# Kernel optimization log

Measured on AMD Instinct MI355X. Metric: run time of the kernel, lower is better.

## Reference

```python
import jax, jax.numpy as jnp
import numpy as np

# 5x5 Sobel kernels (exact constants from the torch module)
_GX5 = np.array([[2.,1.,1e-6,-1.,-2.],[3.,2.,1e-6,-2.,-3.],[4.,3.,0.,-3.,-4.],[3.,2.,1e-6,-2.,-3.],[2.,1.,1e-6,-1.,-2.]], np.float32)
_GY5 = np.array([[2.,3.,4.,3.,2.],[1.,2.,3.,2.,1.],[1e-6,1e-6,1e-6,1e-6,1e-6],[-1.,-2.,-3.,-2.,-1.],[-2.,-3.,-4.,-3.,-2.]], np.float32)


def _sobel(x):  # x: [B,1,H,W] -> [B,2,H,W] (gx, gy)
    k = jnp.stack([jnp.asarray(_GX5), jnp.asarray(_GY5)])[:, None]  # [2,1,5,5]
    return jax.lax.conv_general_dilated(x, k, (1, 1), 'SAME',
                                        dimension_numbers=('NCHW', 'OIHW', 'NCHW'))


def _quantize(gx, gy):
    # OrientQuantize: magnitude + orientation quantized to 8 bins
    div = 3.1416 / 8.0
    mag = jnp.sqrt(gx * gx + gy * gy + 1e-8)
    o = jnp.arctan2(gy, gx)
    conds = [
        (o >= div) & (o < 3 * div),
        (o >= 3 * div) & (o < 5 * div),
        (o >= 5 * div) & (o < 7 * div),
        ((o >= 7 * div) & (o < 8 * div)) | ((o >= -8 * div) & (o < -7 * div)),
        (o >= -7 * div) & (o < -5 * div),
        (o >= -5 * div) & (o < -3 * div),
        (o >= -3 * div) & (o < -div),
        (o >= -div) & (o < div),
    ]
    q = jnp.select(conds, [jnp.full_like(o, float(i)) for i in range(8)], 3.0)
    return mag, q.astype(jnp.int32)


def setup_inputs() -> dict:
    key = jax.random.key(0)
    k1, k2, k3 = jax.random.split(key, 3)
    return {
        'seg_map': jax.random.normal(k1, (2, 21, 256, 256), jnp.float32),
        'dense_ft': jax.random.normal(k2, (2, 256, 256, 256), jnp.float32),
        'mask': jax.random.normal(k3, (2, 21, 256, 256), jnp.float32),
        'label_with_bg': jnp.ones((2, 21), jnp.float32),
    }


def reference(seg_map, dense_ft, mask, label_with_bg):
    BETA, K, STEP = 1000.0, 100, 5
    n, C, h, w = seg_map.shape
    nfg, ch, hw = C - 1, dense_ft.shape[1], h * w

    # ---- Mix_fg: per-class Sobel orientation edges on sharpened softmax ----
    seg = jax.nn.softmax(seg_map * BETA, axis=1)[:, 1:]            # [n,nfg,h,w]
    edges = _sobel(seg.reshape(n * nfg, 1, h, w)).reshape(n, nfg, 2, h, w)
    label_fg = label_with_bg[:, 1:]                                 # [n,nfg]
    edges = edges * label_fg[:, :, None, None, None]
    mag, q = _quantize(edges[:, :, 0], edges[:, :, 1])              # [n,nfg,h,w]

    # ---- boundary pixels: strongest-K edge magnitudes per (b,c) ----
    _, pos = jax.lax.top_k(mag.reshape(n, nfg, hw), K)              # [n,nfg,K]
    o = jnp.take_along_axis(q.reshape(n, nfg, hw), pos, -1) + 1     # 1..8

    # ---- in_out_div: walk STEP pixels along/against gradient orientation ----
    mod4 = ((o % 4) == 0).astype(jnp.int32)
    horiz = ((o == 2) | (o == 6)).astype(jnp.int32)
    p_out = jnp.where(o < 4, STEP * STEP, -STEP)   # (-STEP)**(1+(o<4))
    p_in = jnp.where(o < 4, -STEP, 1)              # (-STEP)**(o<4)
    s_out = jnp.where(o % 2 == 0, -1, 1)           # (-1)**(1+o)
    s_in = -s_out                                   # (-1)**o
    out_idx = pos + p_out * mod4 * w + s_out * horiz
    in_idx = pos + p_in * mod4 * w + s_in * horiz

    def valid(x):
        return (x % (w - 1) != 0) & (x % (w - 1) != 1) & (x > 0) & (x < hw - 1)

    v_out, v_in = valid(out_idx), valid(in_idx)                     # [n,nfg,K] bool
    oi = jnp.clip(out_idx, 0, hw - 1)
    ii = jnp.clip(in_idx, 0, hw - 1)

    # ---- gather features / mask probs at walked positions ----
    dense = jax.nn.softmax(dense_ft, axis=1).reshape(n, ch, hw)
    msk = jax.nn.softmax(mask, axis=1).reshape(n, C, hw)
    b = jnp.arange(n)[:, None, None]
    outs = dense[b, :, oi]                                          # [n,nfg,K,ch]
    ins = jax.lax.stop_gradient(dense[b, :, ii])                    # detached
    outs_m = jax.lax.stop_gradient(msk[b, :, oi])
    ins_m = jax.lax.stop_gradient(msk[b, :, ii])

    sim = jnp.einsum('bcie,bcje->bcij', outs, ins)                  # [n,nfg,K,K]
    sim_m = jnp.einsum('bcie,bcje->bcij', outs_m, ins_m)

    fvi = v_in.astype(sim.dtype)
    fvo = v_out.astype(sim.dtype)
    ci = jnp.maximum(fvi.sum(-1), 1.0)
    co = jnp.maximum(fvo.sum(-1), 1.0)

    def rowmean(s):  # mean over in-samples -> [n,nfg,K]
        return (s * fvi[:, :, None, :]).sum(-1) / ci[..., None]

    def colmean(s):  # mean over out-samples -> [n,nfg,K]
        return (s * fvo[:, :, :, None]).sum(-2) / co[..., None]

    def gmean(s):    # global masked mean -> [n,nfg]
        num = (s * fvo[:, :, :, None] * fvi[:, :, None, :]).sum((-2, -1))
        return num / jnp.maximum(fvo.sum(-1) * fvi.sum(-1), 1.0)

    def beacon(sgn_mask, sgn_dense, vals, v):
        # loss_constructor: signed masked means over FP/FN/TP/TN categories
        def term(cat, sign):
            m = (cat & v).astype(vals.dtype)
            cnt = m.sum(-1)
            return sign * jnp.where(cnt > 0, (vals * m).sum(-1) / jnp.maximum(cnt, 1.0), 0.0)
        FP = sgn_mask & ~sgn_dense
        FN = ~sgn_mask & sgn_dense
        TP = ~sgn_mask & ~sgn_dense
        TN = sgn_mask & sgn_dense
        return term(FP, -1.0) + term(FN, 1.0) + term(TP, 1.0) + term(TN, -1.0)

    g = gmean(sim)
    gm = gmean(sim_m)
    rm, rmm = rowmean(sim), rowmean(sim_m)
    cm, cmm = colmean(sim), colmean(sim_m)
    sgn_rm = jax.lax.stop_gradient(rm) > g[..., None]
    sgn_rmm = rmm > gm[..., None]
    sgn_cm = jax.lax.stop_gradient(cm) > g[..., None]
    sgn_cmm = cmm > gm[..., None]

    loss_bc = beacon(sgn_rmm, sgn_rm, rm, v_out) + beacon(sgn_cmm, sgn_cm, cm, v_in)
    gate = ((v_in.sum(-1) >= 10) & (v_out.sum(-1) >= 10)).astype(loss_bc.dtype)
    gate = gate * (label_fg > 0).astype(loss_bc.dtype)
    return (loss_bc * gate).sum()
```

## Files before the change

### kernel.cpp

```cpp
#include <hip/hip_runtime.h>
#include <math.h>

#define HW 65536
#define WID 256
#define HEI 256
#define NB 2
#define NFG 20
#define NMAP 40
#define CH 256
#define CSEG 21
#define TK 100
#define PARTS 32
#define PARTN (HW / PARTS)
#define RPP (HEI / PARTS)
#define CAND (PARTS * TK)

__device__ __constant__ float c_GX[25] = {
  2.f,1.f,1e-6f,-1.f,-2.f,
  3.f,2.f,1e-6f,-2.f,-3.f,
  4.f,3.f,0.f,-3.f,-4.f,
  3.f,2.f,1e-6f,-2.f,-3.f,
  2.f,1.f,1e-6f,-1.f,-2.f};
__device__ __constant__ float c_GY[25] = {
  2.f,3.f,4.f,3.f,2.f,
  1.f,2.f,3.f,2.f,1.f,
  1e-6f,1e-6f,1e-6f,1e-6f,1e-6f,
  -1.f,-2.f,-3.f,-2.f,-1.f,
  -2.f,-3.f,-4.f,-3.f,-2.f};

__global__ __launch_bounds__(256) void k_seg(const float* __restrict__ seg_map,
                                             double* __restrict__ seg) {
  int idx = blockIdx.x * blockDim.x + threadIdx.x;
  if (idx >= NB * HW) return;
  int b = idx / HW, p = idx % HW;
  double x[CSEG];
  double m = -INFINITY;
  #pragma unroll
  for (int c = 0; c < CSEG; ++c) {
    double v = (double)seg_map[(size_t)(b * CSEG + c) * HW + p] * 1000.0;
    x[c] = v;
    m = fmax(m, v);
  }
  double s = 0.0;
  #pragma unroll
  for (int c = 0; c < CSEG; ++c) {
    double d = x[c] - m;
    double e = (d < -746.0) ? 0.0 : exp(d);
    x[c] = e; s += e;
  }
  #pragma unroll
  for (int c = 1; c < CSEG; ++c)
    seg[(size_t)(b * NFG + (c - 1)) * HW + p] = x[c] / s;
}

__global__ __launch_bounds__(256) void k_sobel_topk(
    const double* __restrict__ seg, const float* __restrict__ label,
    unsigned char* __restrict__ qb,
    unsigned long long* __restrict__ ckey, int* __restrict__ cidx) {
  int mapi = blockIdx.x / PARTS, part = blockIdx.x % PARTS;
  int tid = threadIdx.x;
  int lane = tid & 63, w = tid >> 6;
  int row0 = part * RPP;
  const double* im = seg + (size_t)mapi * HW;

  __shared__ double tile[RPP + 4][WID];
  __shared__ unsigned int hist4[4][256];
  __shared__ int wtot[4];
  __shared__ int s_r, s_cnt, s_bsel;

  for (int r = 0; r < RPP + 4; ++r) {
    int gr = row0 - 2 + r;
    tile[r][tid] = (gr >= 0 && gr < HEI) ? im[gr * WID + tid] : 0.0;
  }
  hist4[0][tid] = 0; hist4[1][tid] = 0; hist4[2][tid] = 0; hist4[3][tid] = 0;
  if (tid == 0) { s_r = TK; s_cnt = 0; }
  __syncthreads();

  int b = mapi / NFG, c = mapi % NFG;
  double lab = (double)label[b * CSEG + c + 1];
  const double DIVQ = 3.1416 / 8.0;
  const double T1 = DIVQ, T3 = 3.0*DIVQ, T5 = 5.0*DIVQ, T7 = 7.0*DIVQ, T8 = 8.0*DIVQ;

  unsigned long long mykey[RPP];
  #pragma unroll
  for (int k = 0; k < RPP; ++k) {
    double gx = 0.0, gy = 0.0;
    #pragma unroll
    for (int dy = 0; dy < 5; ++dy) {
      #pragma unroll
      for (int dx = 0; dx < 5; ++dx) {
        int xx = tid + dx - 2;
        double v = (xx >= 0 && xx < WID) ? tile[k + dy][xx] : 0.0;
        gx += v * (double)c_GX[dy * 5 + dx];
        gy += v * (double)c_GY[dy * 5 + dx];
      }
    }
    gx *= lab; gy *= lab;
    double mg = sqrt(gx * gx + gy * gy + 1e-8);
    double o = atan2(gy, gx);
    int qv;
    if (o >= T1 && o < T3) qv = 0;
    else if (o >= T3 && o < T5) qv = 1;
    else if (o >= T5 && o < T7) qv = 2;
    else if ((o >= T7 && o < T8) || (o >= -T8 && o < -T7)) qv = 3;
    else if (o >= -T7 && o < -T5) qv = 4;
    else if (o >= -T5 && o < -T3) qv = 5;
    else if (o >= -T3 && o < -T1) qv = 6;
    else if (o >= -T1 && o < T1) qv = 7;
    else qv = 3;
    mykey[k] = (unsigned long long)__double_as_longlong(mg);
    qb[(size_t)mapi * HW + (size_t)(row0 + k) * WID + tid] = (unsigned char)qv;
  }
  __syncthreads();
  unsigned long long* sk = (unsigned long long*)&tile[0][0];
  #pragma unroll
  for (int k = 0; k < RPP; ++k) sk[k * WID + tid] = mykey[k];
  __syncthreads();

  unsigned long long pfx = 0ull, msk = 0ull;
  for (int round = 0; round < 8; ++round) {
    int shift = 56 - 8 * round;
    #pragma unroll
    for (int k = 0; k < RPP; ++k) {
      unsigned long long key = mykey[k];
      if ((key & msk) == pfx)
        atomicAdd(&hist4[w][(unsigned int)(key >> shift) & 0xFFu], 1u);
    }
    __syncthreads();
    int r = s_r;
    int cnt = (int)(hist4[0][tid] + hist4[1][tid] + hist4[2][tid] + hist4[3][tid]);
    hist4[0][tid] = 0; hist4[1][tid] = 0; hist4[2][tid] = 0; hist4[3][tid] = 0;
    int v = cnt;
    #pragma unroll
    for (int off = 1; off < 64; off <<= 1) {
      int u = __shfl_down(v, off, 64);
      if (lane + off < 64) v += u;
    }
    if (lane == 0) wtot[w] = v;
    __syncthreads();
    int add = 0;
    for (int ww = w + 1; ww < 4; ++ww) add += wtot[ww];
    v += add;
    if (v >= r && v - cnt < r) { s_bsel = tid; s_r = r - (v - cnt); }
    __syncthreads();
    pfx |= ((unsigned long long)s_bsel << shift);
    msk |= (0xFFull << shift);
  }
  unsigned long long kv = pfx;
  int need_eq = s_r;

  unsigned long long* outk = ckey + (size_t)mapi * CAND + (size_t)part * TK;
  int* outi = cidx + (size_t)mapi * CAND + (size_t)part * TK;
  int gbase = part * PARTN;
  const int CHN = PARTN / 256;
  int base = tid * CHN;
  int myeq = 0;
  for (int k = 0; k < CHN; ++k) {
    unsigned long long key = sk[base + k];
    if (key > kv) {
      int slot = atomicAdd(&s_cnt, 1);
      outk[slot] = key; outi[slot] = gbase + base + k;
    } else if (key == kv) ++myeq;
  }
  int v2 = myeq;
  #pragma unroll
  for (int off = 1; off < 64; off <<= 1) {
    int u = __shfl_up(v2, off, 64);
    if (lane >= off) v2 += u;
  }
  if (lane == 63) wtot[w] = v2;
  __syncthreads();
  int addl = 0;
  for (int ww = 0; ww < w; ++ww) addl += wtot[ww];
  int incl = v2 + addl;
  int rank = incl - myeq;
  int eqtot = wtot[0] + wtot[1] + wtot[2] + wtot[3];
  int lo = eqtot - need_eq;
  int wb = TK - need_eq;
  for (int k = 0; k < CHN; ++k) {
    unsigned long long key = sk[base + k];
    if (key == kv) {
      if (rank >= lo) { outk[wb + rank - lo] = key; outi[wb + rank - lo] = gbase + base + k; }
      ++rank;
    }
  }
}

__global__ __launch_bounds__(256) void k_topk_merge(
    const unsigned long long* __restrict__ ckey,
    const int* __restrict__ cidx, int* __restrict__ pos) {
  int mapi = blockIdx.x, tid = threadIdx.x;
  int lane = tid & 63, w = tid >> 6;
  __shared__ unsigned long long k_[CAND];
  __shared__ int i_[CAND];
  __shared__ int eqi[CAND];
  __shared__ unsigned int hist4[4][256];
  __shared__ int wtot[4];
  __shared__ int s_r, s_cnt, s_eqn, s_bsel;
  for (int c = tid; c < CAND; c += 256) {
    k_[c] = ckey[(size_t)mapi * CAND + c];
    i_[c] = cidx[(size_t)mapi * CAND + c];
  }
  hist4[0][tid] = 0; hist4[1][tid] = 0; hist4[2][tid] = 0; hist4[3][tid] = 0;
  if (tid == 0) { s_r = TK; s_cnt = 0; s_eqn = 0; }
  __syncthreads();
  unsigned long long pfx = 0ull, msk = 0ull;
  for (int round = 0; round < 8; ++round) {
    int shift = 56 - 8 * round;
    for (int c = tid; c < CAND; c += 256) {
      unsigned long long key = k_[c];
      if ((key & msk) == pfx)
        atomicAdd(&hist4[w][(unsigned int)(key >> shift) & 0xFFu], 1u);
    }
    __syncthreads();
    int r = s_r;
    int cnt = (int)(hist4[0][tid] + hist4[1][tid] + hist4[2][tid] + hist4[3][tid]);
    hist4[0][tid] = 0; hist4[1][tid] = 0; hist4[2][tid] = 0; hist4[3][tid] = 0;
    int v = cnt;
    #pragma unroll
    for (int off = 1; off < 64; off <<= 1) {
      int u = __shfl_down(v, off, 64);
      if (lane + off < 64) v += u;
    }
    if (lane == 0) wtot[w] = v;
    __syncthreads();
    int add = 0;
    for (int ww = w + 1; ww < 4; ++ww) add += wtot[ww];
    v += add;
    if (v >= r && v - cnt < r) { s_bsel = tid; s_r = r - (v - cnt); }
    __syncthreads();
    pfx |= ((unsigned long long)s_bsel << shift);
    msk |= (0xFFull << shift);
  }
  unsigned long long kv = pfx;
  int need_eq = s_r;
  for (int c = tid; c < CAND; c += 256) {
    unsigned long long key = k_[c];
    if (key > kv) {
      int slot = atomicAdd(&s_cnt, 1);
      pos[mapi * TK + slot] = i_[c];
    } else if (key == kv) {
      int e = atomicAdd(&s_eqn, 1);
      eqi[e] = i_[c];
    }
  }
  __syncthreads();
  int eqn = s_eqn;
  int wb = TK - need_eq;
  for (int e = tid; e < eqn; e += 256) {
    int myi = eqi[e];
    int bigger = 0;
    for (int f = 0; f < eqn; ++f) bigger += (eqi[f] > myi) ? 1 : 0;
    if (bigger < need_eq) pos[mapi * TK + wb + bigger] = myi;
  }
}

__global__ __launch_bounds__(256) void k_gather(
    const float* __restrict__ dense_ft, const float* __restrict__ maskp,
    const unsigned char* __restrict__ qb, const int* __restrict__ pos,
    double* __restrict__ outs, double* __restrict__ ins,
    double* __restrict__ outs_m, double* __restrict__ ins_m,
    int* __restrict__ voutArr, int* __restrict__ vinArr) {
  int blk = blockIdx.x;
  int mapi = blk / TK, j = blk % TK;
  int b = mapi / NFG;
  int tid = threadIdx.x;
  int lane = tid & 63, w = tid >> 6;
  int p = pos[mapi * TK + j];
  int o = (int)qb[(size_t)mapi * HW + p] + 1;
  int mod4 = ((o & 3) == 0) ? 1 : 0;
  int horiz = (o == 2 || o == 6) ? 1 : 0;
  int po = (o < 4) ? 25 : -5;
  int pi = (o < 4) ? -5 : 1;
  int so = ((o & 1) == 0) ? -1 : 1;
  int si = -so;
  int out_idx = p + po * mod4 * WID + so * horiz;
  int in_idx  = p + pi * mod4 * WID + si * horiz;
  int ro = out_idx % 255; if (ro < 0) ro += 255;
  int ri = in_idx  % 255; if (ri < 0) ri += 255;
  int vo = (ro != 0 && ro != 1 && out_idx > 0 && out_idx < HW - 1) ? 1 : 0;
  int vi = (ri != 0 && ri != 1 && in_idx  > 0 && in_idx  < HW - 1) ? 1 : 0;
  int oi = out_idx < 0 ? 0 : (out_idx > HW - 1 ? HW - 1 : out_idx);
  int ii = in_idx  < 0 ? 0 : (in_idx  > HW - 1 ? HW - 1 : in_idx);
  if (tid == 0) { voutArr[mapi * TK + j] = vo; vinArr[mapi * TK + j] = vi; }

  if (w < 2) {
    int idx = (w == 0) ? oi : ii;
    double x[4];
    double mx = -INFINITY;
    #pragma unroll
    for (int q = 0; q < 4; ++q) {
      x[q] = (double)dense_ft[(size_t)(b * CH + lane + 64 * q) * HW + idx];
      mx = fmax(mx, x[q]);
    }
    #pragma unroll
    for (int off = 1; off < 64; off <<= 1) mx = fmax(mx, __shfl_xor(mx, off, 64));
    double e[4], s = 0.0;
    #pragma unroll
    for (int q = 0; q < 4; ++q) { e[q] = exp(x[q] - mx); s += e[q]; }
    #pragma unroll
    for (int off = 1; off < 64; off <<= 1) s += __shfl_xor(s, off, 64);
    double* dst = ((w == 0) ? outs : ins) + ((size_t)mapi * TK + j) * CH;
    #pragma unroll
    for (int q = 0; q < 4; ++q) dst[lane + 64 * q] = e[q] / s;
  } else {
    int idx = (w == 2) ? oi : ii;
    double y = (lane < CSEG) ? (double)maskp[(size_t)(b * CSEG + lane) * HW + idx]
                             : -INFINITY;
    double mx = y;
    #pragma unroll
    for (int off = 1; off < 64; off <<= 1) mx = fmax(mx, __shfl_xor(mx, off, 64));
    double e = (lane < CSEG) ? exp(y - mx) : 0.0;
    double s = e;
    #pragma unroll
    for (int off = 1; off < 64; off <<= 1) s += __shfl_xor(s, off, 64);
    if (lane < CSEG)
      (((w == 2) ? outs_m : ins_m) + ((size_t)mapi * TK + j) * CSEG)[lane] = e / s;
  }
}

__global__ __launch_bounds__(256) void k_stats(
    const double* __restrict__ outs, const double* __restrict__ ins,
    const double* __restrict__ outs_m, const double* __restrict__ ins_m,
    const int* __restrict__ voutArr, const int* __restrict__ vinArr,
    const float* __restrict__ label, double* __restrict__ lossmap) {
  int mapi = blockIdx.x, tid = threadIdx.x;
  int b = mapi / NFG, c = mapi % NFG;
  __shared__ double fvo[TK], fvi[TK];
  __shared__ double avi[CH], avo[CH], avim[CSEG], avom[CSEG];
  __shared__ double rm[TK], cm[TK], rmm[TK], cmm[TK];
  __shared__ double s_sfvo, s_sfvi;
  if (tid < TK) {
    fvo[tid] = (double)voutArr[mapi * TK + tid];
    fvi[tid] = (double)vinArr[mapi * TK + tid];
  }
  __syncthreads();
  if (tid == 0) {
    double a = 0.0, d = 0.0;
    for (int j2 = 0; j2 < TK; ++j2) { a += fvo[j2]; d += fvi[j2]; }
    s_sfvo = a; s_sfvi = d;
  }
  const double* OUT  = outs   + (size_t)mapi * TK * CH;
  const double* IN   = ins    + (size_t)mapi * TK * CH;
  const double* OUTm = outs_m + (size_t)mapi * TK * CSEG;
  const double* INm  = ins_m  + (size_t)mapi * TK * CSEG;
  {
    double a = 0.0, d = 0.0;
    for (int j2 = 0; j2 < TK; ++j2) {
      a += IN[j2 * CH + tid] * fvi[j2];
      d += OUT[j2 * CH + tid] * fvo[j2];
    }
    avi[tid] = a; avo[tid] = d;
  }
  if (tid < CSEG) {
    double a = 0.0, d = 0.0;
    for (int j2 = 0; j2 < TK; ++j2) {
      a += INm[j2 * CSEG + tid] * fvi[j2];
      d += OUTm[j2 * CSEG + tid] * fvo[j2];
    }
    avim[tid] = a; avom[tid] = d;
  }
  __syncthreads();
  double ci = fmax(s_sfvi, 1.0), co = fmax(s_sfvo, 1.0);
  if (tid < TK) {
    double d1 = 0.0, d2 = 0.0, d3 = 0.0, d4 = 0.0;
    for (int e = 0; e < CH; ++e) { d1 += OUT[tid * CH + e] * avi[e]; d2 += IN[tid * CH + e] * avo[e]; }
    for (int e = 0; e < CSEG; ++e) { d3 += OUTm[tid * CSEG + e] * avim[e]; d4 += INm[tid * CSEG + e] * avom[e]; }
    rm[tid] = d1 / ci; cm[tid] = d2 / co; rmm[tid] = d3 / ci; cmm[tid] = d4 / co;
  }
  __syncthreads();
  if (tid == 0) {
    double g = 0.0, gm = 0.0;
    for (int e = 0; e < CH; ++e) g += avo[e] * avi[e];
    for (int e = 0; e < CSEG; ++e) gm += avom[e] * avim[e];
    double den = fmax(s_sfvo * s_sfvi, 1.0);
    g /= den; gm /= den;
    double loss = 0.0;
    {
      double s[4] = {0, 0, 0, 0}, cn[4] = {0, 0, 0, 0};
      for (int j2 = 0; j2 < TK; ++j2) {
        int smv = rmm[j2] > gm;
        int dmv = rm[j2] > g;
        int cat = smv ? (dmv ? 3 : 0) : (dmv ? 1 : 2);
        s[cat] += rm[j2] * fvo[j2];
        cn[cat] += fvo[j2];
      }
      const double sg[4] = {-1.0, 1.0, 1.0, -1.0};
      for (int t = 0; t < 4; ++t)
        if (cn[t] > 0.0) loss += sg[t] * (s[t] / fmax(cn[t], 1.0));
    }
    {
      double s[4] = {0, 0, 0, 0}, cn[4] = {0, 0, 0, 0};
      for (int j2 = 0; j2 < TK; ++j2) {
        int smv = cmm[j2] > gm;
        int dmv = cm[j2] > g;
        int cat = smv ? (dmv ? 3 : 0) : (dmv ? 1 : 2);
        s[cat] += cm[j2] * fvi[j2];
        cn[cat] += fvi[j2];
      }
      const double sg[4] = {-1.0, 1.0, 1.0, -1.0};
      for (int t = 0; t < 4; ++t)
        if (cn[t] > 0.0) loss += sg[t] * (s[t] / fmax(cn[t], 1.0));
    }
    float lab = label[b * CSEG + c + 1];
    double gate = (s_sfvi >= 10.0 && s_sfvo >= 10.0 && lab > 0.f) ? 1.0 : 0.0;
    lossmap[mapi] = loss * gate;
  }
}

__global__ __launch_bounds__(64) void k_final(const double* __restrict__ lossmap,
                                              float* __restrict__ out) {
  if (threadIdx.x == 0 && blockIdx.x == 0) {
    double s = 0.0;
    for (int i = 0; i < NMAP; ++i) s += lossmap[i];
    out[0] = (float)s;
  }
}

extern "C" void kernel_launch(void* const* d_in, const int* in_sizes, int n_in,
                              void* d_out, int out_size, void* d_ws, size_t ws_size,
                              hipStream_t stream) {
  const float* seg_map  = (const float*)d_in[0];
  const float* dense_ft = (const float*)d_in[1];
  const float* maskp    = (const float*)d_in[2];
  const float* label    = (const float*)d_in[3];
  float* outp = (float*)d_out;

  char* w = (char*)d_ws;
  double* seg = (double*)w;               w += (size_t)NB * NFG * HW * 8;
  double* outs   = (double*)w;            w += (size_t)NMAP * TK * CH * 8;
  double* ins    = (double*)w;            w += (size_t)NMAP * TK * CH * 8;
  double* outs_m = (double*)w;            w += (size_t)NMAP * TK * CSEG * 8;
  double* ins_m  = (double*)w;            w += (size_t)NMAP * TK * CSEG * 8;
  double* lossmap = (double*)w;           w += (size_t)NMAP * 8;
  unsigned long long* ckey = (unsigned long long*)w; w += (size_t)NMAP * CAND * 8;
  int* cidx = (int*)w;                    w += (size_t)NMAP * CAND * 4;
  int* pos  = (int*)w;                    w += (size_t)NMAP * TK * 4;
  int* vout = (int*)w;                    w += (size_t)NMAP * TK * 4;
  int* vin  = (int*)w;                    w += (size_t)NMAP * TK * 4;
  unsigned char* qb = (unsigned char*)w;  w += (size_t)NMAP * HW;

  k_seg<<<(NB * HW + 255) / 256, 256, 0, stream>>>(seg_map, seg);
  k_sobel_topk<<<NMAP * PARTS, 256, 0, stream>>>(seg, label, qb, ckey, cidx);
  k_topk_merge<<<NMAP, 256, 0, stream>>>(ckey, cidx, pos);
  k_gather<<<NMAP * TK, 256, 0, stream>>>(dense_ft, maskp, qb, pos, outs, ins,
                                          outs_m, ins_m, vout, vin);
  k_stats<<<NMAP, 256, 0, stream>>>(outs, ins, outs_m, ins_m, vout, vin, label, lossmap);
  k_final<<<1, 64, 0, stream>>>(lossmap, outp);
}
```

Measured before the change: 199.5 us.

## Speed up radix-select top-k with run-length histogram atomics and early exit

In both the per-part Sobel top-k and the merge kernel, histogram updates now combine consecutive keys that fall in the same bin into one atomic add. Each thread also scans a contiguous chunk of candidates in the merge, so neighbouring keys are more likely to share a bin. The radix rounds stop early once the selected bucket holds a single key. The O(n^2) tie-breaking among equal keys in the merge is replaced by a fast path when all ties are needed, or a two-round radix select on indices. The goal is to cut shared-memory atomic contention and redundant rounds, at the cost of extra branches and a nondeterministic output order for tied entries.

```diff
diff --git a/kernel.cpp b/kernel.cpp
--- a/kernel.cpp
+++ b/kernel.cpp
@@ -14,6 +14,7 @@
 #define PARTN (HW / PARTS)
 #define RPP (HEI / PARTS)
 #define CAND (PARTS * TK)
+#define MCH 13
 
 __device__ __constant__ float c_GX[25] = {
   2.f,1.f,1e-6f,-1.f,-2.f,
@@ -66,7 +67,8 @@
   __shared__ double tile[RPP + 4][WID];
   __shared__ unsigned int hist4[4][256];
   __shared__ int wtot[4];
-  __shared__ int s_r, s_cnt, s_bsel;
+  __shared__ int s_r, s_cnt, s_bsel, s_selcnt;
+  __shared__ unsigned long long s_kv;
 
   for (int r = 0; r < RPP + 4; ++r) {
     int gr = row0 - 2 + r;
@@ -118,14 +120,21 @@
   __syncthreads();
 
   unsigned long long pfx = 0ull, msk = 0ull;
+  int early = 0;
   for (int round = 0; round < 8; ++round) {
     int shift = 56 - 8 * round;
+    int curb = -1; unsigned int curc = 0;
     #pragma unroll
     for (int k = 0; k < RPP; ++k) {
       unsigned long long key = mykey[k];
-      if ((key & msk) == pfx)
-        atomicAdd(&hist4[w][(unsigned int)(key >> shift) & 0xFFu], 1u);
-    }
+      int bk = ((key & msk) == pfx) ? (int)((key >> shift) & 0xFF) : -1;
+      if (bk == curb) { ++curc; }
+      else {
+        if (curb >= 0) atomicAdd(&hist4[w][curb], curc);
+        curb = bk; curc = 1;
+      }
+    }
+    if (curb >= 0) atomicAdd(&hist4[w][curb], curc);
     __syncthreads();
     int r = s_r;
     int cnt = (int)(hist4[0][tid] + hist4[1][tid] + hist4[2][tid] + hist4[3][tid]);
@@ -141,12 +150,22 @@
     int add = 0;
     for (int ww = w + 1; ww < 4; ++ww) add += wtot[ww];
     v += add;
-    if (v >= r && v - cnt < r) { s_bsel = tid; s_r = r - (v - cnt); }
+    if (v >= r && v - cnt < r) { s_bsel = tid; s_r = r - (v - cnt); s_selcnt = cnt; }
     __syncthreads();
     pfx |= ((unsigned long long)s_bsel << shift);
     msk |= (0xFFull << shift);
-  }
-  unsigned long long kv = pfx;
+    if (s_selcnt == 1) { early = 1; break; }
+  }
+  if (early) {
+    #pragma unroll
+    for (int k = 0; k < RPP; ++k)
+      if ((mykey[k] & msk) == pfx) s_kv = mykey[k];
+    __syncthreads();
+  } else {
+    if (tid == 0) s_kv = pfx;
+    __syncthreads();
+  }
+  unsigned long long kv = s_kv;
   int need_eq = s_r;
 
   unsigned long long* outk = ckey + (size_t)mapi * CAND + (size_t)part * TK;
@@ -196,22 +215,35 @@
   __shared__ int eqi[CAND];
   __shared__ unsigned int hist4[4][256];
   __shared__ int wtot[4];
-  __shared__ int s_r, s_cnt, s_eqn, s_bsel;
+  __shared__ int s_r, s_cnt, s_eqn, s_bsel, s_selcnt, s_w2;
+  __shared__ unsigned long long s_kv;
   for (int c = tid; c < CAND; c += 256) {
     k_[c] = ckey[(size_t)mapi * CAND + c];
     i_[c] = cidx[(size_t)mapi * CAND + c];
   }
   hist4[0][tid] = 0; hist4[1][tid] = 0; hist4[2][tid] = 0; hist4[3][tid] = 0;
-  if (tid == 0) { s_r = TK; s_cnt = 0; s_eqn = 0; }
+  if (tid == 0) { s_r = TK; s_cnt = 0; s_eqn = 0; s_w2 = 0; }
   __syncthreads();
   unsigned long long pfx = 0ull, msk = 0ull;
+  int early = 0;
+  int mbase = tid * MCH;
   for (int round = 0; round < 8; ++round) {
     int shift = 56 - 8 * round;
-    for (int c = tid; c < CAND; c += 256) {
-      unsigned long long key = k_[c];
-      if ((key & msk) == pfx)
-        atomicAdd(&hist4[w][(unsigned int)(key >> shift) & 0xFFu], 1u);
-    }
+    int curb = -1; unsigned int curc = 0;
+    for (int t = 0; t < MCH; ++t) {
+      int cc = mbase + t;
+      int bk = -1;
+      if (cc < CAND) {
+        unsigned long long key = k_[cc];
+        if ((key & msk) == pfx) bk = (int)((key >> shift) & 0xFF);
+      }
+      if (bk == curb) { ++curc; }
+      else {
+        if (curb >= 0) atomicAdd(&hist4[w][curb], curc);
+        curb = bk; curc = 1;
+      }
+    }
+    if (curb >= 0) atomicAdd(&hist4[w][curb], curc);
     __syncthreads();
     int r = s_r;
     int cnt = (int)(hist4[0][tid] + hist4[1][tid] + hist4[2][tid] + hist4[3][tid]);
@@ -227,12 +259,21 @@
     int add = 0;
     for (int ww = w + 1; ww < 4; ++ww) add += wtot[ww];
     v += add;
-    if (v >= r && v - cnt < r) { s_bsel = tid; s_r = r - (v - cnt); }
+    if (v >= r && v - cnt < r) { s_bsel = tid; s_r = r - (v - cnt); s_selcnt = cnt; }
     __syncthreads();
     pfx |= ((unsigned long long)s_bsel << shift);
     msk |= (0xFFull << shift);
-  }
-  unsigned long long kv = pfx;
+    if (s_selcnt == 1) { early = 1; break; }
+  }
+  if (early) {
+    for (int c = tid; c < CAND; c += 256)
+      if ((k_[c] & msk) == pfx) s_kv = k_[c];
+    __syncthreads();
+  } else {
+    if (tid == 0) s_kv = pfx;
+    __syncthreads();
+  }
+  unsigned long long kv = s_kv;
   int need_eq = s_r;
   for (int c = tid; c < CAND; c += 256) {
     unsigned long long key = k_[c];
@@ -247,11 +288,46 @@
   __syncthreads();
   int eqn = s_eqn;
   int wb = TK - need_eq;
+  if (eqn == need_eq) {
+    for (int e = tid; e < eqn; e += 256) pos[mapi * TK + wb + e] = eqi[e];
+    return;
+  }
+  if (tid == 0) s_r = need_eq;
+  __syncthreads();
+  unsigned int ipfx = 0u, imsk = 0u;
+  for (int round = 0; round < 2; ++round) {
+    int shift = 8 * (1 - round);
+    for (int e = tid; e < eqn; e += 256) {
+      unsigned int iv = (unsigned int)eqi[e];
+      if ((iv & imsk) == ipfx)
+        atomicAdd(&hist4[w][(iv >> shift) & 0xFFu], 1u);
+    }
+    __syncthreads();
+    int r = s_r;
+    int cnt = (int)(hist4[0][tid] + hist4[1][tid] + hist4[2][tid] + hist4[3][tid]);
+    hist4[0][tid] = 0; hist4[1][tid] = 0; hist4[2][tid] = 0; hist4[3][tid] = 0;
+    int v = cnt;
+    #pragma unroll
+    for (int off = 1; off < 64; off <<= 1) {
+      int u = __shfl_down(v, off, 64);
+      if (lane + off < 64) v += u;
+    }
+    if (lane == 0) wtot[w] = v;
+    __syncthreads();
+    int add = 0;
+    for (int ww = w + 1; ww < 4; ++ww) add += wtot[ww];
+    v += add;
+    if (v >= r && v - cnt < r) { s_bsel = tid; s_r = r - (v - cnt); }
+    __syncthreads();
+    ipfx |= ((unsigned int)s_bsel << shift);
+    imsk |= (0xFFu << shift);
+  }
+  int thrIdx = (int)ipfx;
   for (int e = tid; e < eqn; e += 256) {
-    int myi = eqi[e];
-    int bigger = 0;
-    for (int f = 0; f < eqn; ++f) bigger += (eqi[f] > myi) ? 1 : 0;
-    if (bigger < need_eq) pos[mapi * TK + wb + bigger] = myi;
+    if (eqi[e] >= thrIdx) {
+      int slot = atomicAdd(&s_w2, 1);
+      pos[mapi * TK + wb + slot] = eqi[e];
+    }
   }
 }
 
```

After: 204.6 us. 2.5% more time.
